# Optimization experiments

Hardware: AMD Instinct MI355X
Metric: run time of the kernel (lower is better)

The kernel has to match this reference:

```python
import jax, jax.numpy as jnp
import numpy as np

N_QUBITS = 8
N_LAYERS = 3
B = 32768
IN_F = 512
OUT_F = 512


def _apply_1q(state, G, q):
    # state: (B, 2,...,2) complex64; G: (2,2) shared or (B,2,2) per-sample gate
    s = jnp.moveaxis(state, 1 + q, -1)
    if G.ndim == 3:
        s = jnp.einsum('bij,...j->...i'.replace('...', 'b...').replace('b...ij', 'bij'), G, s) if False else jnp.einsum('bij,b...j->b...i', G, s)
    else:
        s = jnp.einsum('ij,b...j->b...i', G, s)
    return jnp.moveaxis(s, -1, 1 + q)


def _cnot(state, c, t):
    # flip target axis on the control=1 slice
    ca, ta = 1 + c, 1 + t
    s0 = jax.lax.index_in_dim(state, 0, ca, keepdims=True)
    s1 = jax.lax.index_in_dim(state, 1, ca, keepdims=True)
    s1 = jnp.flip(s1, axis=ta)
    return jnp.concatenate([s0, s1], axis=ca)


def _circuit(angles, qparams):
    # angles: (B, 8) RY embedding angles; qparams: (3, 8) RX layer angles
    b = angles.shape[0]
    state = jnp.zeros((b, 2 ** N_QUBITS), dtype=jnp.complex64).at[:, 0].set(1.0)
    state = state.reshape((b,) + (2,) * N_QUBITS)
    # RY(theta) = [[c, -s], [s, c]], per-sample angles
    half = 0.5 * angles
    c, s = jnp.cos(half), jnp.sin(half)
    for q in range(N_QUBITS):
        G = jnp.stack([jnp.stack([c[:, q], -s[:, q]], -1),
                       jnp.stack([s[:, q], c[:, q]], -1)], -2).astype(jnp.complex64)
        state = _apply_1q(state, G, q)
    # layers: RX(params[l,q]) on each wire, then ring of CNOTs
    hp = 0.5 * qparams
    cp, sp = jnp.cos(hp), jnp.sin(hp)
    for l in range(N_LAYERS):
        for q in range(N_QUBITS):
            # RX(theta) = [[c, -i s], [-i s, c]]
            G = jnp.stack([jnp.stack([cp[l, q] + 0j, -1j * sp[l, q]], -1),
                           jnp.stack([-1j * sp[l, q], cp[l, q] + 0j], -1)], -2).astype(jnp.complex64)
            state = _apply_1q(state, G, q)
        for i in range(N_QUBITS - 1):
            state = _cnot(state, i, i + 1)
        state = _cnot(state, N_QUBITS - 1, 0)
    # <Z_q> = P(bit_q=0) - P(bit_q=1)
    probs = jnp.real(state) ** 2 + jnp.imag(state) ** 2
    zs = []
    for q in range(N_QUBITS):
        p = jnp.moveaxis(probs, 1 + q, 1).reshape(b, 2, -1).sum(-1)
        zs.append(p[:, 0] - p[:, 1])
    return jnp.stack(zs, axis=1)  # (B, 8) float32


def setup_inputs() -> dict:
    key = jax.random.key(0)
    k = jax.random.split(key, 6)
    x = jax.random.normal(k[0], (B, IN_F), dtype=jnp.float32)
    fc_w = jax.random.normal(k[1], (N_QUBITS, IN_F), dtype=jnp.float32) / np.sqrt(IN_F)
    fc_b = jax.random.normal(k[2], (N_QUBITS,), dtype=jnp.float32) * 0.01
    qparams = jax.random.normal(k[3], (N_LAYERS, N_QUBITS), dtype=jnp.float32) * 0.1
    post_w = jax.random.normal(k[4], (OUT_F, N_QUBITS), dtype=jnp.float32) / np.sqrt(N_QUBITS)
    post_b = jax.random.normal(k[5], (OUT_F,), dtype=jnp.float32) * 0.01
    return {"x": x, "fc_w": fc_w, "fc_b": fc_b, "qparams": qparams,
            "post_w": post_w, "post_b": post_b}


def reference(x, fc_w, fc_b, qparams, post_w, post_b):
    xproj = x @ fc_w.T + fc_b            # (B, 8) angles
    z = _circuit(xproj, qparams)          # (B, 8) PauliZ expectations
    return z @ post_w.T + post_b          # (B, OUT_F)
```

## Files before the change

### kernel.cpp

```cpp
#include <hip/hip_runtime.h>

#define BLOCK 512
typedef float v2f __attribute__((ext_vector_type(2)));

__device__ __forceinline__ v2f pk_fma(v2f a, v2f b, v2f c) {
  v2f d;
  asm("v_pk_fma_f32 %0, %1, %2, %3" : "=v"(d) : "v"(a), "v"(b), "v"(c));
  return d;
}
__device__ __forceinline__ v2f pk_mul(v2f a, v2f b) {
  v2f d;
  asm("v_pk_mul_f32 %0, %1, %2" : "=v"(d) : "v"(a), "v"(b));
  return d;
}
__device__ __forceinline__ v2f pk_mul_swap(v2f s, v2f p) {
  v2f d;
  asm("v_pk_mul_f32 %0, %1, %2 op_sel:[0,1] op_sel_hi:[1,0]" : "=v"(d) : "v"(s), "v"(p));
  return d;
}

template<int CTRL>
__device__ __forceinline__ float dpp_f(float v) {
  return __int_as_float(__builtin_amdgcn_mov_dpp(__float_as_int(v), CTRL, 0xF, 0xF, true));
}
template<int MASK>
__device__ __forceinline__ float shx(float v) {
  if constexpr (MASK == 1)      return dpp_f<0xB1>(v);
  else if constexpr (MASK == 2) return dpp_f<0x4E>(v);
  else if constexpr (MASK == 8) return dpp_f<0x128>(v);
  else
    return __int_as_float(__builtin_amdgcn_ds_swizzle(__float_as_int(v), 0x101F));
}

__device__ __forceinline__ int gmap(int b) {
#pragma unroll
  for (int j = 0; j < 7; ++j) b ^= ((b >> (j + 1)) & 1) << j;
  b ^= (b & 1) << 7;
  return b;
}

#define MQ_PACKED 0x99CC66B359AC5632ULL

__device__ __forceinline__ void build_w(const float* th, int u, v2f* wr2, float* wup) {
  float uf[8], vf[8];
#pragma unroll
  for (int q = 0; q < 8; ++q) {
    const float h = 0.5f * th[q];
    const float c_ = __cosf(h), s_ = __sinf(h);
    uf[q] = c_ + s_; vf[q] = c_ - s_;
  }
  v2f P01; P01.x = uf[0]; P01.y = vf[0];
  const float r12[4] = {uf[1] * uf[2], vf[1] * uf[2], uf[1] * vf[2], vf[1] * vf[2]};
#pragma unroll
  for (int k = 0; k < 8; ++k) {
    const float rest = r12[k & 3] * ((k & 4) ? vf[3] : uf[3]);
    v2f rr; rr.x = rest; rr.y = rest;
    wr2[k] = pk_mul(P01, rr);
  }
  const bool b4 = (u & 1), b5 = (u & 2), b6 = (u & 4), b7 = (u & 8);
  const float f4 = b4 ? vf[4] : uf[4], g4 = b4 ? uf[4] : vf[4];
  const float f5 = b5 ? vf[5] : uf[5], g5 = b5 ? uf[5] : vf[5];
  const float f6 = b6 ? vf[6] : uf[6], g6 = b6 ? uf[6] : vf[6];
  const float f7 = b7 ? vf[7] : uf[7], g7 = b7 ? uf[7] : vf[7];
  const float A0 = f4 * f5, A1 = g4 * f5, A2 = f4 * g5, A3 = g4 * g5;
  const float B0 = f6 * f7, B1 = g6 * f7, B2 = f6 * g7, B3 = g6 * g7;
  const float wu = A0 * B0;
  wup[0] = wu * (A3 * B0);
  wup[1] = wu * (A1 * B1);
  wup[2] = wu * (A2 * B2);
  wup[3] = wup[1];
  wup[4] = wu * (A3 * B2);
  wup[5] = wu * (A2 * B1);
  wup[6] = wu * (A0 * B3);
  wup[7] = wu * (A1 * B2);
}

template<int Q, int XOR, bool SWAP>
__device__ __forceinline__ void dot1(const float4* kb4, const v2f* wA, const v2f* wB,
                                     float wupA, float wupB, float& zA, float& zB) {
  v2f aA, aB; aA.x = aA.y = 0.f; aB.x = aB.y = 0.f;
#pragma unroll
  for (int k2 = 0; k2 < 4; ++k2) {
    const float4 kv = kb4[(Q * 4 + k2) * 16];
    v2f klo; klo.x = kv.x; klo.y = kv.y;
    v2f khi; khi.x = kv.z; khi.y = kv.w;
    const int k0 = 2 * k2, k1 = 2 * k2 + 1;
    v2f pA0 = SWAP ? pk_mul_swap(wA[k0], wA[k0 ^ XOR]) : pk_mul(wA[k0], wA[k0 ^ XOR]);
    v2f pA1 = SWAP ? pk_mul_swap(wA[k1], wA[k1 ^ XOR]) : pk_mul(wA[k1], wA[k1 ^ XOR]);
    v2f pB0 = SWAP ? pk_mul_swap(wB[k0], wB[k0 ^ XOR]) : pk_mul(wB[k0], wB[k0 ^ XOR]);
    v2f pB1 = SWAP ? pk_mul_swap(wB[k1], wB[k1 ^ XOR]) : pk_mul(wB[k1], wB[k1 ^ XOR]);
    aA = pk_fma(pA0, klo, aA);
    aA = pk_fma(pA1, khi, aA);
    aB = pk_fma(pB0, klo, aB);
    aB = pk_fma(pB1, khi, aB);
  }
  zA = (aA.x + aA.y) * wupA;
  zB = (aB.x + aB.y) * wupB;
}
template<int Q1, int Q2, int XOR, bool SWAP>
__device__ __forceinline__ void dot2(const float4* kb4, const v2f* wA, const v2f* wB,
                                     float wupA1, float wupA2, float wupB1, float wupB2,
                                     float& zA1, float& zA2, float& zB1, float& zB2) {
  v2f a1A, a2A, a1B, a2B;
  a1A.x = a1A.y = a2A.x = a2A.y = 0.f;
  a1B.x = a1B.y = a2B.x = a2B.y = 0.f;
#pragma unroll
  for (int k2 = 0; k2 < 4; ++k2) {
    const float4 kv1 = kb4[(Q1 * 4 + k2) * 16];
    const float4 kv2 = kb4[(Q2 * 4 + k2) * 16];
    v2f k1lo; k1lo.x = kv1.x; k1lo.y = kv1.y;
    v2f k1hi; k1hi.x = kv1.z; k1hi.y = kv1.w;
    v2f k2lo; k2lo.x = kv2.x; k2lo.y = kv2.y;
    v2f k2hi; k2hi.x = kv2.z; k2hi.y = kv2.w;
    const int k0 = 2 * k2, k1 = 2 * k2 + 1;
    v2f pA0 = SWAP ? pk_mul_swap(wA[k0], wA[k0 ^ XOR]) : pk_mul(wA[k0], wA[k0 ^ XOR]);
    v2f pA1 = SWAP ? pk_mul_swap(wA[k1], wA[k1 ^ XOR]) : pk_mul(wA[k1], wA[k1 ^ XOR]);
    v2f pB0 = SWAP ? pk_mul_swap(wB[k0], wB[k0 ^ XOR]) : pk_mul(wB[k0], wB[k0 ^ XOR]);
    v2f pB1 = SWAP ? pk_mul_swap(wB[k1], wB[k1 ^ XOR]) : pk_mul(wB[k1], wB[k1 ^ XOR]);
    a1A = pk_fma(pA0, k1lo, a1A); a1A = pk_fma(pA1, k1hi, a1A);
    a2A = pk_fma(pA0, k2lo, a2A); a2A = pk_fma(pA1, k2hi, a2A);
    a1B = pk_fma(pB0, k1lo, a1B); a1B = pk_fma(pB1, k1hi, a1B);
    a2B = pk_fma(pB0, k2lo, a2B); a2B = pk_fma(pB1, k2hi, a2B);
  }
  zA1 = (a1A.x + a1A.y) * wupA1;
  zA2 = (a2A.x + a2A.y) * wupA2;
  zB1 = (a1B.x + a1B.y) * wupB1;
  zB2 = (a2B.x + a2B.y) * wupB2;
}

__global__ __launch_bounds__(BLOCK, 4) void qcnn_kernel(
    const float* __restrict__ x,   const float* __restrict__ fcw,
    const float* __restrict__ fcb, const float* __restrict__ qp,
    const float* __restrict__ pw,  const float* __restrict__ pb,
    float* __restrict__ out)
{
  __shared__ float s_fcw[8 * 512];
  __shared__ float s_pwt[8 * 512];
  __shared__ float s_pb[512];
  __shared__ float s_beta[256];
  __shared__ float s_K3[8][4][16][4];

  const int tid = threadIdx.x;
  const int wave = tid >> 6;
  const int lane = tid & 63;
  const int u = lane & 15;
  const int g = lane >> 4;

  const int base = blockIdx.x * 64 + wave * 8;
  const int sA = base + g;
  const int sB = base + 4 + g;

  const float* xrA = x + (size_t)sA * 512 + u * 4;
  const float* xrB = x + (size_t)sB * 512 + u * 4;
  float4 xpa[8], xpb[8];
#pragma unroll
  for (int t = 0; t < 8; ++t) xpa[t] = *(const float4*)(xrA + t * 64);
#pragma unroll
  for (int t = 0; t < 8; ++t) xpb[t] = *(const float4*)(xrB + t * 64);

  for (int i = tid; i < 1024; i += BLOCK)
    ((float4*)s_fcw)[i] = ((const float4*)fcw)[i];
  for (int i = tid; i < 1024; i += BLOCK) {
    const float4 v = ((const float4*)pw)[i];
    const int row = i >> 1, c0 = 4 * (i & 1);
    s_pwt[(c0 + 0) * 512 + row] = v.x;
    s_pwt[(c0 + 1) * 512 + row] = v.y;
    s_pwt[(c0 + 2) * 512 + row] = v.z;
    s_pwt[(c0 + 3) * 512 + row] = v.w;
  }
  if (tid < 128) ((float4*)s_pb)[tid] = ((const float4*)pb)[tid];
  if (tid < 256) {
    const int c = tid;
    const int i1 = gmap(c);
    const int i2 = gmap(i1);
    float ang = 0.f;
#pragma unroll
    for (int q = 0; q < 8; ++q) {
      ang += (((c  >> q) & 1) ? 0.5f : -0.5f) * qp[q];
      ang += (((i1 >> q) & 1) ? 0.5f : -0.5f) * qp[8 + q];
      ang += (((i2 >> q) & 1) ? 0.5f : -0.5f) * qp[16 + q];
    }
    s_beta[c] = ang;
  }
  __syncthreads();

  for (int i = tid; i < 2048; i += BLOCK) {
    const int q = i >> 8, c = i & 255;
    const int m = (int)((MQ_PACKED >> (8 * q)) & 0xFF);
    const float kv = __cosf(s_beta[c ^ m] - s_beta[c]) * (1.0f / 256.0f);
    s_K3[q][(c & 15) >> 2][c >> 4][c & 3] = kv;
  }
  __syncthreads();

  v2f accA[8], accB[8];
#pragma unroll
  for (int q = 0; q < 8; ++q) {
    accA[q].x = 0.f; accA[q].y = 0.f;
    accB[q].x = 0.f; accB[q].y = 0.f;
  }
#pragma unroll
  for (int t = 0; t < 8; ++t) {
    const float4 xa = xpa[t];
    const float4 xb = xpb[t];
    v2f xa01; xa01.x = xa.x; xa01.y = xa.y;
    v2f xa23; xa23.x = xa.z; xa23.y = xa.w;
    v2f xb01; xb01.x = xb.x; xb01.y = xb.y;
    v2f xb23; xb23.x = xb.z; xb23.y = xb.w;
#pragma unroll
    for (int q = 0; q < 8; ++q) {
      const float4 wv = *(const float4*)(s_fcw + q * 512 + u * 4 + t * 64);
      v2f w01; w01.x = wv.x; w01.y = wv.y;
      v2f w23; w23.x = wv.z; w23.y = wv.w;
      accA[q] = pk_fma(xa01, w01, accA[q]);
      accA[q] = pk_fma(xa23, w23, accA[q]);
      accB[q] = pk_fma(xb01, w01, accB[q]);
      accB[q] = pk_fma(xb23, w23, accB[q]);
    }
  }
  float thA[8], thB[8];
#pragma unroll
  for (int q = 0; q < 8; ++q) {
    float aA = accA[q].x + accA[q].y;
    float aB = accB[q].x + accB[q].y;
    aA += shx<1>(aA); aB += shx<1>(aB);
    aA += shx<2>(aA); aB += shx<2>(aB);
    aA += shx<4>(aA); aB += shx<4>(aB);
    aA += shx<8>(aA); aB += shx<8>(aB);
    const float fb = fcb[q];
    thA[q] = aA + fb; thB[q] = aB + fb;
  }

  v2f wA[8], wB[8];
  float wupA[8], wupB[8];
  build_w(thA, u, wA, wupA);
  build_w(thB, u, wB, wupB);

  float zpA[8], zpB[8];
  {
    const float4* kb4 = ((const float4*)s_K3) + u;
    dot1<0, 1, false>(kb4, wA, wB, wupA[0], wupB[0], zpA[0], zpB[0]);
    dot1<4, 1, true >(kb4, wA, wB, wupA[4], wupB[4], zpA[4], zpB[4]);
    dot2<1, 5, 3, false>(kb4, wA, wB, wupA[1], wupA[5], wupB[1], wupB[5],
                         zpA[1], zpA[5], zpB[1], zpB[5]);
    dot2<2, 6, 6, false>(kb4, wA, wB, wupA[2], wupA[6], wupB[2], wupB[6],
                         zpA[2], zpA[6], zpB[2], zpB[6]);
    dot2<3, 7, 4, true >(kb4, wA, wB, wupA[3], wupA[7], wupB[3], wupB[7],
                         zpA[3], zpA[7], zpB[3], zpB[7]);
  }
#pragma unroll
  for (int q = 0; q < 8; ++q) { zpA[q] += shx<1>(zpA[q]); zpB[q] += shx<1>(zpB[q]); }
#pragma unroll
  for (int q = 0; q < 8; ++q) { zpA[q] += shx<2>(zpA[q]); zpB[q] += shx<2>(zpB[q]); }
#pragma unroll
  for (int q = 0; q < 8; ++q) { zpA[q] += shx<4>(zpA[q]); zpB[q] += shx<4>(zpB[q]); }
#pragma unroll
  for (int q = 0; q < 8; ++q) { zpA[q] += shx<8>(zpA[q]); zpB[q] += shx<8>(zpB[q]); }

  v2f zzA[8], zzB[8];
#pragma unroll
  for (int q = 0; q < 8; ++q) {
    zzA[q].x = zpA[q]; zzA[q].y = zpA[q];
    zzB[q].x = zpB[q]; zzB[q].y = zpB[q];
  }
  float* orA = out + (size_t)sA * 512;
  float* orB = out + (size_t)sB * 512;
#pragma unroll
  for (int tt = 0; tt < 8; ++tt) {
    const int o = u * 4 + tt * 64;
    const float4 pbv = *(const float4*)(s_pb + o);
    v2f rA0; rA0.x = pbv.x; rA0.y = pbv.y;
    v2f rA1; rA1.x = pbv.z; rA1.y = pbv.w;
    v2f rB0 = rA0, rB1 = rA1;
#pragma unroll
    for (int q = 0; q < 8; ++q) {
      const float4 wv = *(const float4*)(s_pwt + q * 512 + o);
      v2f w01; w01.x = wv.x; w01.y = wv.y;
      v2f w23; w23.x = wv.z; w23.y = wv.w;
      rA0 = pk_fma(zzA[q], w01, rA0);
      rA1 = pk_fma(zzA[q], w23, rA1);
      rB0 = pk_fma(zzB[q], w01, rB0);
      rB1 = pk_fma(zzB[q], w23, rB1);
    }
    float4 ovA; ovA.x = rA0.x; ovA.y = rA0.y; ovA.z = rA1.x; ovA.w = rA1.y;
    float4 ovB; ovB.x = rB0.x; ovB.y = rB0.y; ovB.z = rB1.x; ovB.w = rB1.y;
    *(float4*)(orA + o) = ovA;
    *(float4*)(orB + o) = ovB;
  }
}

extern "C" void kernel_launch(void* const* d_in, const int* in_sizes, int n_in,
                              void* d_out, int out_size, void* d_ws, size_t ws_size,
                              hipStream_t stream) {
  const float* x   = (const float*)d_in[0];
  const float* fcw = (const float*)d_in[1];
  const float* fcb = (const float*)d_in[2];
  const float* qp  = (const float*)d_in[3];
  const float* pw  = (const float*)d_in[4];
  const float* pb  = (const float*)d_in[5];
  float* out = (float*)d_out;

  dim3 grid(512), block(BLOCK);
  hipLaunchKernelGGL(qcnn_kernel, grid, block, 0, stream, x, fcw, fcb, qp, pw, pb, out);
}
```

Baseline: 123.6 us.

## Split fused kernel into quantum-expectation and output-projection kernels

The single fused kernel becomes two. The first projects inputs, simulates the circuit and writes the eight Z expectations per sample into the first slots of that sample's output row. The second kernel loads the transposed post-weights and bias into shared memory, reads those staged Z values back and writes the full 512-wide output. This lowers shared-memory and register pressure in each kernel, which may help occupancy, at the cost of an extra launch, a serialization point between the two kernels and a small extra global round trip.

```diff
diff --git a/kernel.cpp b/kernel.cpp
--- a/kernel.cpp
+++ b/kernel.cpp
@@ -128,15 +128,12 @@
   zB2 = (a2B.x + a2B.y) * wupB2;
 }
 
-__global__ __launch_bounds__(BLOCK, 4) void qcnn_kernel(
+__global__ __launch_bounds__(BLOCK, 4) void qcnn_z(
     const float* __restrict__ x,   const float* __restrict__ fcw,
     const float* __restrict__ fcb, const float* __restrict__ qp,
-    const float* __restrict__ pw,  const float* __restrict__ pb,
     float* __restrict__ out)
 {
   __shared__ float s_fcw[8 * 512];
-  __shared__ float s_pwt[8 * 512];
-  __shared__ float s_pb[512];
   __shared__ float s_beta[256];
   __shared__ float s_K3[8][4][16][4];
 
@@ -160,15 +157,6 @@
 
   for (int i = tid; i < 1024; i += BLOCK)
     ((float4*)s_fcw)[i] = ((const float4*)fcw)[i];
-  for (int i = tid; i < 1024; i += BLOCK) {
-    const float4 v = ((const float4*)pw)[i];
-    const int row = i >> 1, c0 = 4 * (i & 1);
-    s_pwt[(c0 + 0) * 512 + row] = v.x;
-    s_pwt[(c0 + 1) * 512 + row] = v.y;
-    s_pwt[(c0 + 2) * 512 + row] = v.z;
-    s_pwt[(c0 + 3) * 512 + row] = v.w;
-  }
-  if (tid < 128) ((float4*)s_pb)[tid] = ((const float4*)pb)[tid];
   if (tid < 256) {
     const int c = tid;
     const int i1 = gmap(c);
@@ -256,14 +244,64 @@
 #pragma unroll
   for (int q = 0; q < 8; ++q) { zpA[q] += shx<8>(zpA[q]); zpB[q] += shx<8>(zpB[q]); }
 
-  v2f zzA[8], zzB[8];
-#pragma unroll
-  for (int q = 0; q < 8; ++q) {
-    zzA[q].x = zpA[q]; zzA[q].y = zpA[q];
-    zzB[q].x = zpB[q]; zzB[q].y = zpB[q];
-  }
+  if (u == 0) {
+    float4 z0, z1;
+    z0.x = zpA[0]; z0.y = zpA[1]; z0.z = zpA[2]; z0.w = zpA[3];
+    z1.x = zpA[4]; z1.y = zpA[5]; z1.z = zpA[6]; z1.w = zpA[7];
+    *(float4*)(out + (size_t)sA * 512)     = z0;
+    *(float4*)(out + (size_t)sA * 512 + 4) = z1;
+    z0.x = zpB[0]; z0.y = zpB[1]; z0.z = zpB[2]; z0.w = zpB[3];
+    z1.x = zpB[4]; z1.y = zpB[5]; z1.z = zpB[6]; z1.w = zpB[7];
+    *(float4*)(out + (size_t)sB * 512)     = z0;
+    *(float4*)(out + (size_t)sB * 512 + 4) = z1;
+  }
+}
+
+__global__ __launch_bounds__(BLOCK, 4) void qcnn_out(
+    const float* __restrict__ pw, const float* __restrict__ pb,
+    float* out)
+{
+  __shared__ float s_pwt[8 * 512];
+  __shared__ float s_pb[512];
+
+  const int tid = threadIdx.x;
+  for (int i = tid; i < 1024; i += BLOCK) {
+    const float4 v = ((const float4*)pw)[i];
+    const int row = i >> 1, c0 = 4 * (i & 1);
+    s_pwt[(c0 + 0) * 512 + row] = v.x;
+    s_pwt[(c0 + 1) * 512 + row] = v.y;
+    s_pwt[(c0 + 2) * 512 + row] = v.z;
+    s_pwt[(c0 + 3) * 512 + row] = v.w;
+  }
+  if (tid < 128) ((float4*)s_pb)[tid] = ((const float4*)pb)[tid];
+  __syncthreads();
+
+  const int wave = tid >> 6;
+  const int lane = tid & 63;
+  const int u = lane & 15;
+  const int g = lane >> 4;
+
+  const int base = blockIdx.x * 64 + wave * 8;
+  const int sA = base + g;
+  const int sB = base + 4 + g;
+
   float* orA = out + (size_t)sA * 512;
   float* orB = out + (size_t)sB * 512;
+
+  const float4 zA0 = *(const float4*)(orA);
+  const float4 zA1 = *(const float4*)(orA + 4);
+  const float4 zB0 = *(const float4*)(orB);
+  const float4 zB1 = *(const float4*)(orB + 4);
+
+  v2f zzA[8], zzB[8];
+  const float zAv[8] = {zA0.x, zA0.y, zA0.z, zA0.w, zA1.x, zA1.y, zA1.z, zA1.w};
+  const float zBv[8] = {zB0.x, zB0.y, zB0.z, zB0.w, zB1.x, zB1.y, zB1.z, zB1.w};
+#pragma unroll
+  for (int q = 0; q < 8; ++q) {
+    zzA[q].x = zAv[q]; zzA[q].y = zAv[q];
+    zzB[q].x = zBv[q]; zzB[q].y = zBv[q];
+  }
+
 #pragma unroll
   for (int tt = 0; tt < 8; ++tt) {
     const int o = u * 4 + tt * 64;
@@ -300,5 +338,6 @@
   float* out = (float*)d_out;
 
   dim3 grid(512), block(BLOCK);
-  hipLaunchKernelGGL(qcnn_kernel, grid, block, 0, stream, x, fcw, fcb, qp, pw, pb, out);
-}
+  hipLaunchKernelGGL(qcnn_z,   grid, block, 0, stream, x, fcw, fcb, qp, out);
+  hipLaunchKernelGGL(qcnn_out, grid, block, 0, stream, pw, pb, out);
+}
```

Result: slower. 132.2 us (+6.9%).
